# Optimization experiments

Measured on AMD Instinct MI355X. Metric: run time of the kernel, lower is better.

The kernel has to match this reference:

```python
import jax, jax.numpy as jnp
import numpy as np

ALPHA = 0.2  # LeakyReLU negative slope


def gat_layer(x, W, a, alpha=ALPHA):
    """Multi-head dense GAT layer.
    x: (B, N, F); W: (H, F, O); a: (H, 2*O, 1).
    Returns (B, N, H*O) — ELU(head outputs) concatenated over heads.
    """
    H, F, O = W.shape
    Wh = jnp.einsum('bnf,hfo->bhno', x, W)          # (B,H,N,O)
    a_src = a[:, :O, 0]                              # (H,O)
    a_dst = a[:, O:, 0]                              # (H,O)
    s_src = jnp.einsum('bhno,ho->bhn', Wh, a_src)    # (B,H,N)
    s_dst = jnp.einsum('bhno,ho->bhn', Wh, a_dst)    # (B,H,N)
    e = s_src[..., :, None] + s_dst[..., None, :]    # (B,H,N,N)
    e = jax.nn.leaky_relu(e, negative_slope=alpha)
    att = jax.nn.softmax(e, axis=-1)                 # softmax over neighbors j
    out = jnp.einsum('bhnm,bhmo->bhno', att, Wh)     # (B,H,N,O)
    out = jax.nn.elu(out)
    B, _, N, _ = out.shape
    return jnp.transpose(out, (0, 2, 1, 3)).reshape(B, N, H * O)


def setup_inputs() -> dict:
    key = jax.random.key(0)
    ks = jax.random.split(key, 5)
    B, N = 32, 1024
    x = jax.random.normal(ks[0], (B, N, 4), dtype=jnp.float32)
    # layer1: nfeat=4, nhid=2, nheads=3
    W1 = jax.random.normal(ks[1], (3, 4, 2), dtype=jnp.float32) * 0.5
    a1 = jax.random.normal(ks[2], (3, 4, 1), dtype=jnp.float32) * 0.5
    # layer2: nfeat=6, nhid=4, nheads=1
    W2 = jax.random.normal(ks[3], (1, 6, 4), dtype=jnp.float32) * 0.5
    a2 = jax.random.normal(ks[4], (1, 8, 1), dtype=jnp.float32) * 0.5
    return {"x": x, "W1": W1, "a1": a1, "W2": W2, "a2": a2}


def reference(x, W1, a1, W2, a2):
    h = gat_layer(x, W1, a1)   # (B, N, 6)
    y = gat_layer(h, W2, a2)   # (B, N, 4)
    return y
```

## Files before the change

kernel.cpp:

```cpp
#include <hip/hip_runtime.h>


#define GAT_ALPHA 0.2f
#define LOG2E 1.44269504088896f

__device__ __forceinline__ float ex2(float v) { return __builtin_amdgcn_exp2f(v); }

constexpr int N = 1024, NT = 1024, NW = NT / 64, NB = 256, BPL = NB / 64;
constexpr int WCS = NB + 1;

constexpr int OFF_KEY = WCS;
constexpr int OFF_WH0 = OFF_KEY + N;
constexpr int OFF_WH1 = OFF_WH0 + N;
constexpr int OFF_PRE = OFF_WH1 + N;
constexpr int OFF_SUF = OFF_PRE + 3 * WCS;
constexpr int L1_HEAD = OFF_SUF + 3 * WCS;
constexpr int SMEM_WORDS = 3 * L1_HEAD;

constexpr int OFF2_KEY = 0;
constexpr int OFF2_WHS = N;
constexpr int OFF2_PRE = OFF2_WHS + 4 * N;
constexpr int OFF2_SUF = OFF2_PRE + 5 * WCS;
constexpr int L2_TOTAL = OFF2_SUF + 5 * WCS;
static_assert(L2_TOTAL <= SMEM_WORDS, "L2 must alias inside L1 region");

__device__ __forceinline__ void wave_scan_int(int* a, int ln) {
    int c[BPL];
#pragma unroll
    for (int i = 0; i < BPL; ++i) c[i] = a[ln * BPL + i];
    int s = 0;
#pragma unroll
    for (int i = 0; i < BPL; ++i) s += c[i];
    int run = s;
#pragma unroll
    for (int d = 1; d < 64; d <<= 1) {
        const int u = __shfl_up(run, d, 64);
        if (ln >= d) run += u;
    }
    int acc = run - s;
#pragma unroll
    for (int i = 0; i < BPL; ++i) { const int t = acc; acc += c[i]; a[ln * BPL + i] = t; }
    if (ln == 63) a[NB] = run;
}
__device__ __forceinline__ void wave_scan_pre(float* a, int ln) {
    float c[BPL];
#pragma unroll
    for (int i = 0; i < BPL; ++i) c[i] = a[ln * BPL + i];
    float s = 0.0f;
#pragma unroll
    for (int i = 0; i < BPL; ++i) s += c[i];
    float run = s;
#pragma unroll
    for (int d = 1; d < 64; d <<= 1) {
        const float u = __shfl_up(run, d, 64);
        if (ln >= d) run += u;
    }
    float acc = run - s;
#pragma unroll
    for (int i = 0; i < BPL; ++i) { const float t = acc; acc += c[i]; a[ln * BPL + i] = t; }
}
__device__ __forceinline__ void wave_scan_suf(float* a, int ln) {
    float c[BPL];
#pragma unroll
    for (int i = 0; i < BPL; ++i) c[i] = a[ln * BPL + i];
    float s = 0.0f;
#pragma unroll
    for (int i = 0; i < BPL; ++i) s += c[i];
    float run = s;
#pragma unroll
    for (int d = 1; d < 64; d <<= 1) {
        const float u = __shfl_down(run, d, 64);
        if (ln < 64 - d) run += u;
    }
    float acc = run - s;
#pragma unroll
    for (int i = BPL - 1; i >= 0; --i) { acc += c[i]; a[ln * BPL + i] = acc; }
}

__global__ __launch_bounds__(NT) void gat_fused(
    const float* __restrict__ x,
    const float* __restrict__ W1,
    const float* __restrict__ a1,
    const float* __restrict__ W2,
    const float* __restrict__ a2,
    float* __restrict__ out)
{
    __shared__ __align__(16) float smem[SMEM_WORDS];
    __shared__ int   cs2[WCS];
    __shared__ float sMM[4][2 * NW];

    const int b   = blockIdx.x;
    const int tid = threadIdx.x, wv = tid >> 6, ln = tid & 63;
    const int m   = tid;

    float Wl1[3][4][2], as1[3][2], ad1[3][2];
#pragma unroll
    for (int hh = 0; hh < 3; ++hh) {
#pragma unroll
        for (int f = 0; f < 4; ++f)
#pragma unroll
            for (int o = 0; o < 2; ++o) Wl1[hh][f][o] = W1[(hh * 4 + f) * 2 + o];
#pragma unroll
        for (int o = 0; o < 2; ++o) {
            as1[hh][o] = a1[hh * 4 + o];
            ad1[hh][o] = a1[hh * 4 + 2 + o];
        }
    }
    float Wl2[6][4], as2[4], ad2[4];
#pragma unroll
    for (int f = 0; f < 6; ++f)
#pragma unroll
        for (int o = 0; o < 4; ++o) Wl2[f][o] = W2[f * 4 + o];
#pragma unroll
    for (int o = 0; o < 4; ++o) { as2[o] = a2[o]; ad2[o] = a2[4 + o]; }

#pragma unroll
    for (int hh = 0; hh < 3; ++hh)
        if (tid < WCS) ((int*)(smem + hh * L1_HEAD))[tid] = 0;
    if (tid < WCS) cs2[tid] = 0;

    const float4 xr = ((const float4*)(x + (size_t)b * N * 4))[m];
    float key1[3], sn1[3], wh1[3][2];
#pragma unroll
    for (int hh = 0; hh < 3; ++hh) {
        const float w0 = xr.x * Wl1[hh][0][0] + xr.y * Wl1[hh][1][0] +
                         xr.z * Wl1[hh][2][0] + xr.w * Wl1[hh][3][0];
        const float w1 = xr.x * Wl1[hh][0][1] + xr.y * Wl1[hh][1][1] +
                         xr.z * Wl1[hh][2][1] + xr.w * Wl1[hh][3][1];
        wh1[hh][0] = w0; wh1[hh][1] = w1;
        key1[hh] = w0 * ad1[hh][0] + w1 * ad1[hh][1];
        sn1[hh]  = w0 * as1[hh][0] + w1 * as1[hh][1];
        float mn = key1[hh], mx = key1[hh];
#pragma unroll
        for (int d = 1; d < 64; d <<= 1) {
            mn = fminf(mn, __shfl_xor(mn, d, 64));
            mx = fmaxf(mx, __shfl_xor(mx, d, 64));
        }
        if (ln == 0) { sMM[hh][wv] = mn; sMM[hh][NW + wv] = mx; }
    }
    __syncthreads();

    float kmin1[3], invw1[3];
#pragma unroll
    for (int hh = 0; hh < 3; ++hh) {
        float mn = sMM[hh][0], mx = sMM[hh][NW];
#pragma unroll
        for (int w = 1; w < NW; ++w) {
            mn = fminf(mn, sMM[hh][w]);
            mx = fmaxf(mx, sMM[hh][NW + w]);
        }
        kmin1[hh] = mn;
        invw1[hh] = (float)NB / fmaxf(mx - mn, 1e-30f);
    }

    int bk1[3], rk1[3];
#pragma unroll
    for (int hh = 0; hh < 3; ++hh) {
        int q = (int)((key1[hh] - kmin1[hh]) * invw1[hh]);
        q = q < 0 ? 0 : (q > NB - 1 ? NB - 1 : q);
        bk1[hh] = q;
        rk1[hh] = atomicAdd((int*)(smem + hh * L1_HEAD) + q, 1);
    }
    __syncthreads();

    if (wv < 3) wave_scan_int((int*)(smem + wv * L1_HEAD), ln);
    __syncthreads();

#pragma unroll
    for (int hh = 0; hh < 3; ++hh) {
        float* bp = smem + hh * L1_HEAD;
        const int pos = ((int*)bp)[bk1[hh]] + rk1[hh];
        bp[OFF_KEY + pos] = key1[hh];
        bp[OFF_WH0 + pos] = wh1[hh][0];
        bp[OFF_WH1 + pos] = wh1[hh][1];
    }
    __syncthreads();

    if (tid < 3 * NB) {
        const int hh = tid >> 8, q = tid & (NB - 1);
        float* bp = smem + hh * L1_HEAD;
        const int i0 = ((const int*)bp)[q], i1 = ((const int*)bp)[q + 1];
        float se1 = 0.0f, se2 = 0.0f, se1w0 = 0.0f, se1w1 = 0.0f, se2w0 = 0.0f, se2w1 = 0.0f;
        for (int i = i0; i < i1; ++i) {
            const float k = bp[OFF_KEY + i];
            const float w0 = bp[OFF_WH0 + i], w1 = bp[OFF_WH1 + i];
            const float e1 = ex2(LOG2E * k);
            const float e2 = ex2(GAT_ALPHA * LOG2E * k);
            se1 += e1; se2 += e2;
            se1w0 += e1 * w0; se1w1 += e1 * w1;
            se2w0 += e2 * w0; se2w1 += e2 * w1;
        }
        bp[OFF_SUF + q] = se1;
        bp[OFF_SUF + WCS + q] = se1w0;
        bp[OFF_SUF + 2 * WCS + q] = se1w1;
        bp[OFF_PRE + q] = se2;
        bp[OFF_PRE + WCS + q] = se2w0;
        bp[OFF_PRE + 2 * WCS + q] = se2w1;
    }
    if (tid < 9) {
        const int hh = tid / 3, a = tid % 3;
        (smem + hh * L1_HEAD)[OFF_SUF + a * WCS + NB] = 0.0f;
    }
    __syncthreads();

    for (int job = wv; job < 18; job += NW) {
        const int hh = job / 6, r = job % 6;
        float* bp = smem + hh * L1_HEAD;
        if (r < 3) wave_scan_pre(bp + OFF_PRE + r * WCS, ln);
        else       wave_scan_suf(bp + OFF_SUF + (r - 3) * WCS, ln);
    }
    __syncthreads();

    float hv[6];
#pragma unroll
    for (int hh = 0; hh < 3; ++hh) {
        float* bp = smem + hh * L1_HEAD;
        const int* cs = (const int*)bp;
        const float sn = sn1[hh];
        const float rho = ex2(0.8f * LOG2E * sn);
        int bq = (int)((-sn - kmin1[hh]) * invw1[hh]);
        bq = bq < 0 ? 0 : (bq > NB - 1 ? NB - 1 : bq);
        const int i0 = cs[bq], i1 = cs[bq + 1];
        float den = rho * bp[OFF_SUF + bq + 1] + bp[OFF_PRE + bq];
        float n0  = rho * bp[OFF_SUF + WCS + bq + 1] + bp[OFF_PRE + WCS + bq];
        float n1  = rho * bp[OFF_SUF + 2 * WCS + bq + 1] + bp[OFF_PRE + 2 * WCS + bq];
        for (int i = i0; i < i1; ++i) {
            const float kk = bp[OFF_KEY + i];
            const float w = fmaxf(rho * ex2(LOG2E * kk), ex2(GAT_ALPHA * LOG2E * kk));
            den += w;
            n0 += w * bp[OFF_WH0 + i];
            n1 += w * bp[OFF_WH1 + i];
        }
        float v0 = n0 / den, v1 = n1 / den;
        hv[hh * 2]     = (v0 > 0.0f) ? v0 : (__expf(v0) - 1.0f);
        hv[hh * 2 + 1] = (v1 > 0.0f) ? v1 : (__expf(v1) - 1.0f);
    }
    float key2, sn2, wh2[4];
    {
        float kd = 0.0f, sn = 0.0f;
#pragma unroll
        for (int o = 0; o < 4; ++o) {
            float acc = 0.0f;
#pragma unroll
            for (int f = 0; f < 6; ++f) acc += hv[f] * Wl2[f][o];
            wh2[o] = acc;
            kd += acc * ad2[o];
            sn += acc * as2[o];
        }
        key2 = kd; sn2 = sn;
        float mn = kd, mx = kd;
#pragma unroll
        for (int d = 1; d < 64; d <<= 1) {
            mn = fminf(mn, __shfl_xor(mn, d, 64));
            mx = fmaxf(mx, __shfl_xor(mx, d, 64));
        }
        if (ln == 0) { sMM[3][wv] = mn; sMM[3][NW + wv] = mx; }
    }
    __syncthreads();

    float kmin2, invw2;
    {
        float mn = sMM[3][0], mx = sMM[3][NW];
#pragma unroll
        for (int w = 1; w < NW; ++w) {
            mn = fminf(mn, sMM[3][w]);
            mx = fmaxf(mx, sMM[3][NW + w]);
        }
        kmin2 = mn;
        invw2 = (float)NB / fmaxf(mx - mn, 1e-30f);
    }

    int bk2, rk2;
    {
        int q = (int)((key2 - kmin2) * invw2);
        q = q < 0 ? 0 : (q > NB - 1 ? NB - 1 : q);
        bk2 = q;
        rk2 = atomicAdd(cs2 + q, 1);
    }
    __syncthreads();

    if (wv == 0) wave_scan_int(cs2, ln);
    __syncthreads();

    {
        const int pos = cs2[bk2] + rk2;
        smem[OFF2_KEY + pos] = key2;
#pragma unroll
        for (int o = 0; o < 4; ++o) smem[OFF2_WHS + o * N + pos] = wh2[o];
    }
    __syncthreads();

    if (tid < NB) {
        const int q = tid;
        const int i0 = cs2[q], i1 = cs2[q + 1];
        float se1 = 0.0f, se2 = 0.0f, se1w[4] = {0, 0, 0, 0}, se2w[4] = {0, 0, 0, 0};
        for (int i = i0; i < i1; ++i) {
            const float k = smem[OFF2_KEY + i];
            const float e1 = ex2(LOG2E * k);
            const float e2 = ex2(GAT_ALPHA * LOG2E * k);
            se1 += e1; se2 += e2;
#pragma unroll
            for (int o = 0; o < 4; ++o) {
                const float w = smem[OFF2_WHS + o * N + i];
                se1w[o] += e1 * w;
                se2w[o] += e2 * w;
            }
        }
        smem[OFF2_SUF + q] = se1;
        smem[OFF2_PRE + q] = se2;
#pragma unroll
        for (int o = 0; o < 4; ++o) {
            smem[OFF2_SUF + (1 + o) * WCS + q] = se1w[o];
            smem[OFF2_PRE + (1 + o) * WCS + q] = se2w[o];
        }
    }
    if (tid >= NB && tid < NB + 5)
        smem[OFF2_SUF + (tid - NB) * WCS + NB] = 0.0f;
    __syncthreads();

    if (wv < 10) {
        if (wv < 5) wave_scan_pre(smem + OFF2_PRE + wv * WCS, ln);
        else        wave_scan_suf(smem + OFF2_SUF + (wv - 5) * WCS, ln);
    }
    __syncthreads();

    {
        const float rho = ex2(0.8f * LOG2E * sn2);
        int bq = (int)((-sn2 - kmin2) * invw2);
        bq = bq < 0 ? 0 : (bq > NB - 1 ? NB - 1 : bq);
        const int i0 = cs2[bq], i1 = cs2[bq + 1];
        float den = rho * smem[OFF2_SUF + bq + 1] + smem[OFF2_PRE + bq];
        float num[4];
#pragma unroll
        for (int o = 0; o < 4; ++o)
            num[o] = rho * smem[OFF2_SUF + (1 + o) * WCS + bq + 1] +
                     smem[OFF2_PRE + (1 + o) * WCS + bq];
        for (int i = i0; i < i1; ++i) {
            const float kk = smem[OFF2_KEY + i];
            const float w = fmaxf(rho * ex2(LOG2E * kk), ex2(GAT_ALPHA * LOG2E * kk));
            den += w;
#pragma unroll
            for (int o = 0; o < 4; ++o) num[o] += w * smem[OFF2_WHS + o * N + i];
        }
        float vv[4];
#pragma unroll
        for (int o = 0; o < 4; ++o) {
            float v = num[o] / den;
            vv[o] = (v > 0.0f) ? v : (__expf(v) - 1.0f);
        }
        float4 yv;
        yv.x = vv[0]; yv.y = vv[1]; yv.z = vv[2]; yv.w = vv[3];
        ((float4*)out)[(size_t)b * N + m] = yv;
    }
}

extern "C" void kernel_launch(void* const* d_in, const int* in_sizes, int n_in,
                              void* d_out, int out_size, void* d_ws, size_t ws_size,
                              hipStream_t stream) {
    const float* x  = (const float*)d_in[0];
    const float* W1 = (const float*)d_in[1];
    const float* a1 = (const float*)d_in[2];
    const float* W2 = (const float*)d_in[3];
    const float* a2 = (const float*)d_in[4];
    float* y = (float*)d_out;

    (void)d_ws; (void)ws_size;
    gat_fused<<<32, NT, 0, stream>>>(x, W1, a1, W2, a2, y);
}
```

Before: 78.81 us.

## Fuse per-bucket exp-sum reduction into wave scan jobs, dropping a barrier

```diff
diff --git a/kernel.cpp b/kernel.cpp
--- a/kernel.cpp
+++ b/kernel.cpp
@@ -42,13 +42,26 @@
     for (int i = 0; i < BPL; ++i) { const int t = acc; acc += c[i]; a[ln * BPL + i] = t; }
     if (ln == 63) a[NB] = run;
 }
-__device__ __forceinline__ void wave_scan_pre(float* a, int ln) {
-    float c[BPL];
-#pragma unroll
-    for (int i = 0; i < BPL; ++i) c[i] = a[ln * BPL + i];
+
+template <bool HASMUL>
+__device__ __forceinline__ void scan_job_pre(const int* cs, const float* keys,
+                                             const float* mul, float escale,
+                                             float* dst, int ln) {
+    float v[BPL];
+#pragma unroll
+    for (int i = 0; i < BPL; ++i) {
+        const int q = ln * BPL + i;
+        const int i0 = cs[q], i1 = cs[q + 1];
+        float s = 0.0f;
+        for (int j = i0; j < i1; ++j) {
+            const float e = ex2(escale * keys[j]);
+            s += HASMUL ? e * mul[j] : e;
+        }
+        v[i] = s;
+    }
     float s = 0.0f;
 #pragma unroll
-    for (int i = 0; i < BPL; ++i) s += c[i];
+    for (int i = 0; i < BPL; ++i) s += v[i];
     float run = s;
 #pragma unroll
     for (int d = 1; d < 64; d <<= 1) {
@@ -57,15 +70,27 @@
     }
     float acc = run - s;
 #pragma unroll
-    for (int i = 0; i < BPL; ++i) { const float t = acc; acc += c[i]; a[ln * BPL + i] = t; }
-}
-__device__ __forceinline__ void wave_scan_suf(float* a, int ln) {
-    float c[BPL];
-#pragma unroll
-    for (int i = 0; i < BPL; ++i) c[i] = a[ln * BPL + i];
+    for (int i = 0; i < BPL; ++i) { const float t = acc; acc += v[i]; dst[ln * BPL + i] = t; }
+}
+template <bool HASMUL>
+__device__ __forceinline__ void scan_job_suf(const int* cs, const float* keys,
+                                             const float* mul, float escale,
+                                             float* dst, int ln) {
+    float v[BPL];
+#pragma unroll
+    for (int i = 0; i < BPL; ++i) {
+        const int q = ln * BPL + i;
+        const int i0 = cs[q], i1 = cs[q + 1];
+        float s = 0.0f;
+        for (int j = i0; j < i1; ++j) {
+            const float e = ex2(escale * keys[j]);
+            s += HASMUL ? e * mul[j] : e;
+        }
+        v[i] = s;
+    }
     float s = 0.0f;
 #pragma unroll
-    for (int i = 0; i < BPL; ++i) s += c[i];
+    for (int i = 0; i < BPL; ++i) s += v[i];
     float run = s;
 #pragma unroll
     for (int d = 1; d < 64; d <<= 1) {
@@ -74,7 +99,8 @@
     }
     float acc = run - s;
 #pragma unroll
-    for (int i = BPL - 1; i >= 0; --i) { acc += c[i]; a[ln * BPL + i] = acc; }
+    for (int i = BPL - 1; i >= 0; --i) { acc += v[i]; dst[ln * BPL + i] = acc; }
+    if (ln == 63) dst[NB] = 0.0f;
 }
 
 __global__ __launch_bounds__(NT) void gat_fused(
@@ -114,10 +140,11 @@
 #pragma unroll
     for (int o = 0; o < 4; ++o) { as2[o] = a2[o]; ad2[o] = a2[4 + o]; }
 
-#pragma unroll
-    for (int hh = 0; hh < 3; ++hh)
-        if (tid < WCS) ((int*)(smem + hh * L1_HEAD))[tid] = 0;
-    if (tid < WCS) cs2[tid] = 0;
+    if (tid < WCS) {
+#pragma unroll
+        for (int hh = 0; hh < 3; ++hh) ((int*)(smem + hh * L1_HEAD))[tid] = 0;
+        cs2[tid] = 0;
+    }
 
     const float4 xr = ((const float4*)(x + (size_t)b * N * 4))[m];
     float key1[3], sn1[3], wh1[3][2];
@@ -176,38 +203,19 @@
     }
     __syncthreads();
 
-    if (tid < 3 * NB) {
-        const int hh = tid >> 8, q = tid & (NB - 1);
-        float* bp = smem + hh * L1_HEAD;
-        const int i0 = ((const int*)bp)[q], i1 = ((const int*)bp)[q + 1];
-        float se1 = 0.0f, se2 = 0.0f, se1w0 = 0.0f, se1w1 = 0.0f, se2w0 = 0.0f, se2w1 = 0.0f;
-        for (int i = i0; i < i1; ++i) {
-            const float k = bp[OFF_KEY + i];
-            const float w0 = bp[OFF_WH0 + i], w1 = bp[OFF_WH1 + i];
-            const float e1 = ex2(LOG2E * k);
-            const float e2 = ex2(GAT_ALPHA * LOG2E * k);
-            se1 += e1; se2 += e2;
-            se1w0 += e1 * w0; se1w1 += e1 * w1;
-            se2w0 += e2 * w0; se2w1 += e2 * w1;
-        }
-        bp[OFF_SUF + q] = se1;
-        bp[OFF_SUF + WCS + q] = se1w0;
-        bp[OFF_SUF + 2 * WCS + q] = se1w1;
-        bp[OFF_PRE + q] = se2;
-        bp[OFF_PRE + WCS + q] = se2w0;
-        bp[OFF_PRE + 2 * WCS + q] = se2w1;
-    }
-    if (tid < 9) {
-        const int hh = tid / 3, a = tid % 3;
-        (smem + hh * L1_HEAD)[OFF_SUF + a * WCS + NB] = 0.0f;
-    }
-    __syncthreads();
-
     for (int job = wv; job < 18; job += NW) {
         const int hh = job / 6, r = job % 6;
         float* bp = smem + hh * L1_HEAD;
-        if (r < 3) wave_scan_pre(bp + OFF_PRE + r * WCS, ln);
-        else       wave_scan_suf(bp + OFF_SUF + (r - 3) * WCS, ln);
+        const int* cs = (const int*)bp;
+        const float* keys = bp + OFF_KEY;
+        switch (r) {
+        case 0: scan_job_pre<false>(cs, keys, nullptr,      GAT_ALPHA * LOG2E, bp + OFF_PRE,           ln); break;
+        case 1: scan_job_pre<true >(cs, keys, bp + OFF_WH0, GAT_ALPHA * LOG2E, bp + OFF_PRE + WCS,     ln); break;
+        case 2: scan_job_pre<true >(cs, keys, bp + OFF_WH1, GAT_ALPHA * LOG2E, bp + OFF_PRE + 2 * WCS, ln); break;
+        case 3: scan_job_suf<false>(cs, keys, nullptr,      LOG2E,             bp + OFF_SUF,           ln); break;
+        case 4: scan_job_suf<true >(cs, keys, bp + OFF_WH0, LOG2E,             bp + OFF_SUF + WCS,     ln); break;
+        default:scan_job_suf<true >(cs, keys, bp + OFF_WH1, LOG2E,             bp + OFF_SUF + 2 * WCS, ln); break;
+        }
     }
     __syncthreads();
 
@@ -290,37 +298,14 @@
     }
     __syncthreads();
 
-    if (tid < NB) {
-        const int q = tid;
-        const int i0 = cs2[q], i1 = cs2[q + 1];
-        float se1 = 0.0f, se2 = 0.0f, se1w[4] = {0, 0, 0, 0}, se2w[4] = {0, 0, 0, 0};
-        for (int i = i0; i < i1; ++i) {
-            const float k = smem[OFF2_KEY + i];
-            const float e1 = ex2(LOG2E * k);
-            const float e2 = ex2(GAT_ALPHA * LOG2E * k);
-            se1 += e1; se2 += e2;
-#pragma unroll
-            for (int o = 0; o < 4; ++o) {
-                const float w = smem[OFF2_WHS + o * N + i];
-                se1w[o] += e1 * w;
-                se2w[o] += e2 * w;
-            }
-        }
-        smem[OFF2_SUF + q] = se1;
-        smem[OFF2_PRE + q] = se2;
-#pragma unroll
-        for (int o = 0; o < 4; ++o) {
-            smem[OFF2_SUF + (1 + o) * WCS + q] = se1w[o];
-            smem[OFF2_PRE + (1 + o) * WCS + q] = se2w[o];
-        }
-    }
-    if (tid >= NB && tid < NB + 5)
-        smem[OFF2_SUF + (tid - NB) * WCS + NB] = 0.0f;
-    __syncthreads();
-
     if (wv < 10) {
-        if (wv < 5) wave_scan_pre(smem + OFF2_PRE + wv * WCS, ln);
-        else        wave_scan_suf(smem + OFF2_SUF + (wv - 5) * WCS, ln);
+        const float* keys = smem + OFF2_KEY;
+        if (wv == 0)     scan_job_pre<false>(cs2, keys, nullptr, GAT_ALPHA * LOG2E, smem + OFF2_PRE, ln);
+        else if (wv < 5) scan_job_pre<true >(cs2, keys, smem + OFF2_WHS + (wv - 1) * N,
+                                             GAT_ALPHA * LOG2E, smem + OFF2_PRE + wv * WCS, ln);
+        else if (wv == 5) scan_job_suf<false>(cs2, keys, nullptr, LOG2E, smem + OFF2_SUF, ln);
+        else              scan_job_suf<true >(cs2, keys, smem + OFF2_WHS + (wv - 6) * N,
+                                              LOG2E, smem + OFF2_SUF + (wv - 5) * WCS, ln);
     }
     __syncthreads();
 
```

After: 84.52 us. +7.2%, slower.
